# Kernel tuning notes

Measured on AMD Instinct MI355X. Metric: run time of the kernel, lower is better.

The kernel has to match this reference:

```python
import jax, jax.numpy as jnp
import numpy as np

T, WS, SHIFT, HEADS, DIM = 5, (8, 8), (4, 4), 6, 192
HEAD_DIM = DIM // HEADS
SCALE = HEAD_DIM ** -0.5
MLP_HID = 4 * DIM
TABLE_LEN = (T * 2 * WS[0] - 1) * (2 * WS[1] - 1)


def _rel_index():
    # exact replica of WindowAttention.__init__ index construction (t,h,w coords)
    ct, ch, cw = np.arange(T), np.arange(WS[0]), np.arange(WS[1])
    coords = np.stack(np.meshgrid(ct, ch, cw, indexing='ij')).reshape(3, -1)
    rel = (coords[:, :, None] - coords[:, None, :]).transpose(1, 2, 0).astype(np.int64)
    rel[:, :, 0] += WS[0] - 1
    rel[:, :, 1] += WS[1] - 1
    rel[:, :, 0] *= 2 * WS[1] - 1
    return jnp.asarray(rel.sum(-1))  # (N, N)


def _attn_mask(H, W):
    # standard shifted-window mask on (H,W); identical across T, so tile (T,T)
    img = np.zeros((H, W), np.float32)
    cnt = 0
    for hs in (slice(0, -WS[0]), slice(-WS[0], -SHIFT[0]), slice(-SHIFT[0], None)):
        for ws_ in (slice(0, -WS[1]), slice(-WS[1], -SHIFT[1]), slice(-SHIFT[1], None)):
            img[hs, ws_] = cnt
            cnt += 1
    img = img.reshape(H // WS[0], WS[0], W // WS[1], WS[1]).transpose(0, 2, 1, 3)
    img = img.reshape(-1, WS[0] * WS[1])  # (nW, Wh*Ww)
    m = img[:, None, :] - img[:, :, None]
    m = np.where(m != 0, -100.0, 0.0).astype(np.float32)
    return jnp.asarray(np.tile(m, (1, T, T)))  # (nW, T*Wh*Ww, T*Wh*Ww)


def _win_part(x, ws):
    B, t, H, W, C = x.shape
    x = x.reshape(B, t, H // ws[0], ws[0], W // ws[1], ws[1], C)
    return x.transpose(0, 2, 4, 1, 3, 5, 6).reshape(-1, t * ws[0] * ws[1], C)


def _win_rev(w, ws, H, W, t, B):
    x = w.reshape(B, H // ws[0], W // ws[1], t, ws[0], ws[1], -1)
    return x.transpose(0, 3, 1, 4, 2, 5, 6).reshape(B, t, H, W, -1)


def _ln(x, g, b):
    mu = x.mean(-1, keepdims=True)
    var = ((x - mu) ** 2).mean(-1, keepdims=True)
    return (x - mu) * jax.lax.rsqrt(var + 1e-5) * g + b


def _forward(x, ln1_g, ln1_b, qkv_w, qkv_b, rel_bias_table, proj_w, proj_b,
             ln2_g, ln2_b, fc1_w, fc1_b, fc2_w, fc2_b, H, W):
    B, L, C = x.shape
    shortcut = x
    h = _ln(x, ln1_g, ln1_b)
    qkv = h @ qkv_w.T + qkv_b                                   # (B, L, 3C)
    qkv = qkv.reshape(B, T, H, W, 3 * C)
    qkv = jnp.roll(qkv, (-SHIFT[0], -SHIFT[1]), axis=(2, 3))
    qkv = _win_part(qkv, WS)                                    # (B_, N, 3C)
    B_, N, _ = qkv.shape
    qkv = qkv.reshape(B_, N, 3, HEADS, HEAD_DIM).transpose(2, 0, 3, 1, 4)
    q, k, v = qkv[0], qkv[1], qkv[2]
    attn = jnp.einsum('bhnd,bhmd->bhnm', q * SCALE, k)          # (B_, H, N, N)
    bias = rel_bias_table[_rel_index()].transpose(2, 0, 1)      # (heads, N, N)
    attn = attn + bias[None]
    mask = _attn_mask(H, W)                                     # (nW, N, N)
    nW = mask.shape[0]
    attn = attn.reshape(B_ // nW, nW, HEADS, N, N) + mask[None, :, None]
    attn = jax.nn.softmax(attn.reshape(B_, HEADS, N, N), axis=-1)
    out = jnp.einsum('bhnm,bhmd->bhnd', attn, v)
    out = out.transpose(0, 2, 1, 3).reshape(B_, N, C)
    out = out @ proj_w.T + proj_b
    out = _win_rev(out, WS, H, W, T, B)
    out = jnp.roll(out, (SHIFT[0], SHIFT[1]), axis=(2, 3)).reshape(B, L, C)
    x = shortcut + out
    h = _ln(x, ln2_g, ln2_b)
    h = jax.nn.gelu(h @ fc1_w.T + fc1_b, approximate=False) @ fc2_w.T + fc2_b
    return x + h


def setup_inputs() -> dict:
    key = jax.random.key(0)
    ks = jax.random.split(key, 8)
    B, Himg, Wimg = 2, 64, 64
    L = T * Himg * Wimg
    s = 0.02
    return {
        'x': jax.random.normal(ks[0], (B, L, DIM), jnp.float32),
        'ln1_g': jnp.ones((DIM,), jnp.float32),
        'ln1_b': jnp.zeros((DIM,), jnp.float32),
        'qkv_w': jax.random.normal(ks[1], (3 * DIM, DIM), jnp.float32) * s,
        'qkv_b': jnp.zeros((3 * DIM,), jnp.float32),
        'rel_bias_table': jax.random.normal(ks[2], (TABLE_LEN, HEADS), jnp.float32) * s,
        'proj_w': jax.random.normal(ks[3], (DIM, DIM), jnp.float32) * s,
        'proj_b': jnp.zeros((DIM,), jnp.float32),
        'ln2_g': jnp.ones((DIM,), jnp.float32),
        'ln2_b': jnp.zeros((DIM,), jnp.float32),
        'fc1_w': jax.random.normal(ks[4], (MLP_HID, DIM), jnp.float32) * s,
        'fc1_b': jnp.zeros((MLP_HID,), jnp.float32),
        'fc2_w': jax.random.normal(ks[5], (DIM, MLP_HID), jnp.float32) * s,
        'fc2_b': jnp.zeros((DIM,), jnp.float32),
        'H': Himg,
        'W': Wimg,
    }


def reference(x, ln1_g, ln1_b, qkv_w, qkv_b, rel_bias_table, proj_w, proj_b,
              ln2_g, ln2_b, fc1_w, fc1_b, fc2_w, fc2_b, H, W):
    return _forward(x, ln1_g, ln1_b, qkv_w, qkv_b, rel_bias_table, proj_w, proj_b,
                    ln2_g, ln2_b, fc1_w, fc1_b, fc2_w, fc2_b, H, W)
```

## Files before the change

### kernel.cpp

```cpp
#include <hip/hip_runtime.h>
#include <math.h>

typedef unsigned short u16;
typedef unsigned int u32;
typedef short bf16x8 __attribute__((ext_vector_type(8)));
typedef float f32x4 __attribute__((ext_vector_type(4)));
typedef _Float16 f16x4 __attribute__((ext_vector_type(4)));

#define TT 5
#define HEADS 6
#define HD 32
#define DIM 192
#define NWIN 320
#define LTOK (TT*64*64)
#define BATCH 2
#define MROWS (BATCH*LTOK)
#define QSCALE 0.17677669529663687f
#define LOG2E 1.4426950408889634f
#define QSCALE2 (QSCALE * LOG2E)
#define MASK2 (-100.0f * LOG2E)

__device__ __forceinline__ u16 f2bf(float f) {
    u32 u = __float_as_uint(f);
    u32 r = (u + 0x7FFFu + ((u >> 16) & 1u)) >> 16;
    return (u16)r;
}
__device__ __forceinline__ float bflo(u32 u) { return __uint_as_float(u << 16); }
__device__ __forceinline__ float bfhi(u32 u) { return __uint_as_float(u & 0xFFFF0000u); }
__device__ __forceinline__ u32 pkh(float a, float b) {
    auto h = __builtin_amdgcn_cvt_pkrtz(a, b);
    return __builtin_bit_cast(u32, h);
}
#if __has_builtin(__builtin_amdgcn_exp2f)
__device__ __forceinline__ float ex2(float x) { return __builtin_amdgcn_exp2f(x); }
#else
__device__ __forceinline__ float ex2(float x) {
    float r; asm("v_exp_f32 %0, %1" : "=v"(r) : "v"(x)); return r;
}
#endif

__global__ __launch_bounds__(256) void cvt4_kernel(
    const float* __restrict__ a, const float* __restrict__ b,
    const float* __restrict__ c, const float* __restrict__ d,
    u16* __restrict__ oa, u16* __restrict__ ob,
    u16* __restrict__ oc, u16* __restrict__ od)
{
    int i = blockIdx.x * 256 + threadIdx.x;
    if (i < 110592)       oa[i]          = f2bf(a[i]);
    else if (i < 147456)  ob[i - 110592] = f2bf(b[i - 110592]);
    else if (i < 294912)  oc[i - 147456] = f2bf(c[i - 147456]);
    else                  od[i - 294912] = f2bf(d[i - 294912]);
}

__global__ __launch_bounds__(256) void ln_kernel(
    const float* __restrict__ x, const float* __restrict__ g,
    const float* __restrict__ b, u16* __restrict__ out)
{
    int tok  = blockIdx.x * 4 + (threadIdx.x >> 6);
    int lane = threadIdx.x & 63;
    const float* xr = x + (size_t)tok * DIM;
    float v0 = xr[lane], v1 = xr[lane + 64], v2 = xr[lane + 128];
    float s = v0 + v1 + v2;
    #pragma unroll
    for (int off = 32; off; off >>= 1) s += __shfl_xor(s, off, 64);
    float mu = s * (1.0f / 192.0f);
    float d0 = v0 - mu, d1 = v1 - mu, d2 = v2 - mu;
    float vs = d0 * d0 + d1 * d1 + d2 * d2;
    #pragma unroll
    for (int off = 32; off; off >>= 1) vs += __shfl_xor(vs, off, 64);
    float rstd = rsqrtf(vs * (1.0f / 192.0f) + 1e-5f);
    u16* orow = out + (size_t)tok * DIM;
    orow[lane]       = f2bf(d0 * rstd * g[lane]       + b[lane]);
    orow[lane + 64]  = f2bf(d1 * rstd * g[lane + 64]  + b[lane + 64]);
    orow[lane + 128] = f2bf(d2 * rstd * g[lane + 128] + b[lane + 128]);
}

template<int EPI, int BM>
__global__ __launch_bounds__(256) void mfma_gemm(
    const u16* __restrict__ A, const u16* __restrict__ W,
    const float* __restrict__ bias, void* __restrict__ outp,
    const float* __restrict__ xin, int N, int K)
{
    constexpr int WR = BM / 64;
    constexpr int NA = BM / 32;
    __shared__ u16 As[BM * 64];
    __shared__ u16 Bs[64 * 64];
    const int tid  = threadIdx.x;
    const int lane = tid & 63, wv = tid >> 6;
    const int ln16 = lane & 15, quad = lane >> 4;

    const int flat  = blockIdx.y * gridDim.x + blockIdx.x;
    const int cpx   = (gridDim.x * gridDim.y) >> 3;
    const int nf    = (flat & 7) * cpx + (flat >> 3);
    const int bn    = nf % gridDim.x;
    const int bm    = nf / gridDim.x;

    const int srow = lane >> 3;
    const int sxor = (lane & 7) ^ srow;
    const int acol = sxor * 8;

    f32x4 acc[WR][4] = {};

    for (int k0 = 0; k0 < K; k0 += 64) {
        __syncthreads();
        #pragma unroll
        for (int a = 0; a < NA; ++a) {
            const u16* g = A + (size_t)(bm * BM + a * 32 + wv * 8 + srow) * K + k0 + acol;
            __builtin_amdgcn_global_load_lds(
                (const __attribute__((address_space(1))) u32*)g,
                (__attribute__((address_space(3))) u32*)((char*)As + a * 4096 + wv * 1024),
                16, 0, 0);
        }
        #pragma unroll
        for (int bb = 0; bb < 2; ++bb) {
            const u16* g = W + (size_t)(bn * 64 + bb * 32 + wv * 8 + srow) * K + k0 + acol;
            __builtin_amdgcn_global_load_lds(
                (const __attribute__((address_space(1))) u32*)g,
                (__attribute__((address_space(3))) u32*)((char*)Bs + bb * 4096 + wv * 1024),
                16, 0, 0);
        }
        __syncthreads();
        #pragma unroll
        for (int s = 0; s < 2; ++s) {
            bf16x8 af[WR], bf[4];
            #pragma unroll
            for (int i = 0; i < WR; ++i) {
                int r = wv * (16 * WR) + i * 16 + ln16;
                int slot = (s * 4 + quad) ^ (r & 7);
                af[i] = *(const bf16x8*)((const char*)As + r * 128 + slot * 16);
            }
            #pragma unroll
            for (int j = 0; j < 4; ++j) {
                int r = j * 16 + ln16;
                int slot = (s * 4 + quad) ^ (r & 7);
                bf[j] = *(const bf16x8*)((const char*)Bs + r * 128 + slot * 16);
            }
            #pragma unroll
            for (int i = 0; i < WR; ++i)
                #pragma unroll
                for (int j = 0; j < 4; ++j)
                    acc[i][j] = __builtin_amdgcn_mfma_f32_16x16x32_bf16(
                        af[i], bf[j], acc[i][j], 0, 0, 0);
        }
    }

    #pragma unroll
    for (int i = 0; i < WR; ++i) {
        int gr0 = bm * BM + wv * (16 * WR) + i * 16 + quad * 4;
        #pragma unroll
        for (int j = 0; j < 4; ++j) {
            int gc = bn * 64 + j * 16 + ln16;
            float bv = bias[gc];
            #pragma unroll
            for (int rr = 0; rr < 4; ++rr) {
                int gr = gr0 + rr;
                float val = acc[i][j][rr] + bv;
                if (EPI == 0) {
                    ((u16*)outp)[(size_t)gr * N + gc] = f2bf(val);
                } else if (EPI == 1) {
                    float gl = val * 0.5f * (1.0f + erff(val * 0.70710678118654752f));
                    ((u16*)outp)[(size_t)gr * N + gc] = f2bf(gl);
                } else if (EPI == 2) {
                    int b_ = gr / NWIN, n = gr - b_ * NWIN;
                    int b = b_ >> 6, hb = (b_ >> 3) & 7, wb = b_ & 7;
                    int t = n >> 6, hi = (n >> 3) & 7, wj = n & 7;
                    int hs = (hb * 8 + hi + 4) & 63;
                    int wsrc = (wb * 8 + wj + 4) & 63;
                    size_t dst = ((size_t)b * LTOK + t * 4096 + hs * 64 + wsrc) * DIM + gc;
                    ((float*)outp)[dst] = xin[dst] + val;
                } else {
                    ((float*)outp)[(size_t)gr * N + gc] += val;
                }
            }
        }
    }
}

__global__ __launch_bounds__(320) void attn_kernel(
    const u16* __restrict__ qkv, const float* __restrict__ table,
    u16* __restrict__ attout)
{
    const int head = blockIdx.x % HEADS;
    const int b_   = blockIdx.x / HEADS;
    const int b = b_ >> 6, hb = (b_ >> 3) & 7, wb = b_ & 7;
    const int tid = threadIdx.x;
    const int lane = tid & 63, wv = tid >> 6;
    const int ln16 = lane & 15, quad = lane >> 4;

    __shared__ u16 Ks[320 * 40];
    __shared__ u16 Vt[32 * 328];
    __shared__ u16 meta[320];
    __shared__ float tbl[188];

    {
        int n = tid;
        int t1 = n >> 6, r1 = (n >> 3) & 7, c1 = n & 7;
        int h1 = hb * 8 + r1, w1 = wb * 8 + c1;
        int l1 = t1 * 4096 + ((h1 + 4) & 63) * 64 + ((w1 + 4) & 63);
        const u16* src = qkv + ((size_t)b * LTOK + l1) * (3 * DIM) + head * HD;
        const uint4* k4 = (const uint4*)(src + DIM);
        #pragma unroll
        for (int i = 0; i < 4; ++i)
            *(uint4*)(Ks + n * 40 + i * 8) = k4[i];
        const uint4* v4 = (const uint4*)(src + 2 * DIM);
        #pragma unroll
        for (int i = 0; i < 4; ++i) {
            uint4 u = v4[i];
            u32 ws[4] = {u.x, u.y, u.z, u.w};
            #pragma unroll
            for (int j = 0; j < 4; ++j) {
                u32 hb2 = pkh(bflo(ws[j]), bfhi(ws[j]));
                int d = i * 8 + j * 2;
                Vt[d * 328 + n]       = (u16)(hb2 & 0xFFFF);
                Vt[(d + 1) * 328 + n] = (u16)(hb2 >> 16);
            }
        }
        int off = (7 - t1) * 15 + 7 - r1 - c1;
        int rh = h1 < 56 ? 0 : (h1 < 60 ? 1 : 2);
        int rw = w1 < 56 ? 0 : (w1 < 60 ? 1 : 2);
        meta[n] = (u16)(off | ((rh * 3 + rw) << 8));
        if (n < 187) tbl[n] = table[n * HEADS + head] * LOG2E;
    }

    bf16x8 qf[4];
    int basen[4], myreg[4];
    #pragma unroll
    for (int qt = 0; qt < 4; ++qt) {
        int nq = wv * 64 + qt * 16 + ln16;
        int t1 = nq >> 6, r1 = (nq >> 3) & 7, c1 = nq & 7;
        int h1 = hb * 8 + r1, w1 = wb * 8 + c1;
        int l1 = t1 * 4096 + ((h1 + 4) & 63) * 64 + ((w1 + 4) & 63);
        qf[qt] = *(const bf16x8*)(qkv + ((size_t)b * LTOK + l1) * (3 * DIM)
                                  + head * HD + quad * 8);
        basen[qt] = t1 * 15 + r1 + c1;
        int rh = h1 < 56 ? 0 : (h1 < 60 ? 1 : 2);
        int rw = w1 < 56 ? 0 : (w1 < 60 ? 1 : 2);
        myreg[qt] = rh * 3 + rw;
    }

    __syncthreads();

    f32x4 o[4][2] = {};
    float l_[4] = {};
    const f32x4 zero = {};

    #pragma unroll 1
    for (int c = 0; c < 10; ++c) {
        int kb = c * 32;
        bf16x8 af0 = *(const bf16x8*)(Ks + (kb + ln16) * 40 + quad * 8);
        bf16x8 af1 = *(const bf16x8*)(Ks + (kb + 16 + ln16) * 40 + quad * 8);
        f16x4 va[2][2];
        #pragma unroll
        for (int dt = 0; dt < 2; ++dt)
            #pragma unroll
            for (int kt = 0; kt < 2; ++kt)
                va[dt][kt] = *(const f16x4*)(Vt + (dt * 16 + ln16) * 328
                                             + kb + kt * 16 + quad * 4);
        ushort4 m4a = *(const ushort4*)(meta + kb + quad * 4);
        ushort4 m4b = *(const ushort4*)(meta + kb + 16 + quad * 4);
        u16 mta[4] = {m4a.x, m4a.y, m4a.z, m4a.w};
        u16 mtb[4] = {m4b.x, m4b.y, m4b.z, m4b.w};

        #pragma unroll
        for (int qt = 0; qt < 4; ++qt) {
            f32x4 s0 = __builtin_amdgcn_mfma_f32_16x16x32_bf16(af0, qf[qt], zero, 0, 0, 0);
            f32x4 s1 = __builtin_amdgcn_mfma_f32_16x16x32_bf16(af1, qf[qt], zero, 0, 0, 0);
            float p[8];
            #pragma unroll
            for (int r = 0; r < 4; ++r) {
                int ma = mta[r], mb = mtb[r];
                float va0 = fmaf(s0[r], QSCALE2, tbl[basen[qt] + (ma & 0xFF)]);
                float vb0 = fmaf(s1[r], QSCALE2, tbl[basen[qt] + (mb & 0xFF)]);
                p[r]     = va0 + (((ma >> 8) == myreg[qt]) ? 0.0f : MASK2);
                p[4 + r] = vb0 + (((mb >> 8) == myreg[qt]) ? 0.0f : MASK2);
            }
            float ls = 0.0f;
            #pragma unroll
            for (int j = 0; j < 8; ++j) { p[j] = ex2(p[j]); ls += p[j]; }
            l_[qt] += ls;
            uint2 pk0 = { pkh(p[0], p[1]), pkh(p[2], p[3]) };
            uint2 pk1 = { pkh(p[4], p[5]), pkh(p[6], p[7]) };
            f16x4 pf0 = __builtin_bit_cast(f16x4, pk0);
            f16x4 pf1 = __builtin_bit_cast(f16x4, pk1);
            #pragma unroll
            for (int dt = 0; dt < 2; ++dt) {
                o[qt][dt] = __builtin_amdgcn_mfma_f32_16x16x16f16(va[dt][0], pf0, o[qt][dt], 0, 0, 0);
                o[qt][dt] = __builtin_amdgcn_mfma_f32_16x16x16f16(va[dt][1], pf1, o[qt][dt], 0, 0, 0);
            }
        }
    }

    #pragma unroll
    for (int qt = 0; qt < 4; ++qt) {
        float lt = l_[qt];
        lt += __shfl_xor(lt, 16, 64);
        lt += __shfl_xor(lt, 32, 64);
        float inv = 1.0f / lt;
        int nq = wv * 64 + qt * 16 + ln16;
        u16* dst = attout + ((size_t)(b_ * NWIN + nq)) * DIM + head * HD + quad * 4;
        #pragma unroll
        for (int dt = 0; dt < 2; ++dt) {
            u32 w0 = (u32)f2bf(o[qt][dt][0] * inv) | ((u32)f2bf(o[qt][dt][1] * inv) << 16);
            u32 w1 = (u32)f2bf(o[qt][dt][2] * inv) | ((u32)f2bf(o[qt][dt][3] * inv) << 16);
            uint2 st = {w0, w1};
            *(uint2*)(dst + dt * 16) = st;
        }
    }
}

extern "C" void kernel_launch(void* const* d_in, const int* in_sizes, int n_in,
                              void* d_out, int out_size, void* d_ws, size_t ws_size,
                              hipStream_t stream)
{
    (void)in_sizes; (void)n_in; (void)out_size; (void)ws_size;
    const float* x      = (const float*)d_in[0];
    const float* ln1_g  = (const float*)d_in[1];
    const float* ln1_b  = (const float*)d_in[2];
    const float* qkv_w  = (const float*)d_in[3];
    const float* qkv_b  = (const float*)d_in[4];
    const float* table  = (const float*)d_in[5];
    const float* proj_w = (const float*)d_in[6];
    const float* proj_b = (const float*)d_in[7];
    const float* ln2_g  = (const float*)d_in[8];
    const float* ln2_b  = (const float*)d_in[9];
    const float* fc1_w  = (const float*)d_in[10];
    const float* fc1_b  = (const float*)d_in[11];
    const float* fc2_w  = (const float*)d_in[12];
    const float* fc2_b  = (const float*)d_in[13];
    float* out = (float*)d_out;

    u16* wsu     = (u16*)d_ws;
    u16* h_buf   = wsu;
    u16* qkv_buf = wsu + (size_t)MROWS * DIM;
    u16* att_buf = wsu + (size_t)MROWS * (4 * DIM);
    u16* fc1_buf = wsu + (size_t)MROWS * DIM;
    u16* wq = wsu + (size_t)MROWS * (5 * DIM);
    u16* wp = wq + 3 * DIM * DIM;
    u16* w1 = wp + DIM * DIM;
    u16* w2 = w1 + 4 * DIM * DIM;

    cvt4_kernel<<<(12 * DIM * DIM) / 256, 256, 0, stream>>>(
        qkv_w, proj_w, fc1_w, fc2_w, wq, wp, w1, w2);

    ln_kernel<<<MROWS / 4, 256, 0, stream>>>(x, ln1_g, ln1_b, h_buf);
    mfma_gemm<0, 128><<<dim3(3 * DIM / 64, MROWS / 128), 256, 0, stream>>>(
        h_buf, wq, qkv_b, qkv_buf, nullptr, 3 * DIM, DIM);
    attn_kernel<<<128 * HEADS, 320, 0, stream>>>(qkv_buf, table, att_buf);
    mfma_gemm<2, 64><<<dim3(DIM / 64, MROWS / 64), 256, 0, stream>>>(
        att_buf, wp, proj_b, out, x, DIM, DIM);
    ln_kernel<<<MROWS / 4, 256, 0, stream>>>(out, ln2_g, ln2_b, h_buf);
    mfma_gemm<1, 128><<<dim3(4 * DIM / 64, MROWS / 128), 256, 0, stream>>>(
        h_buf, w1, fc1_b, fc1_buf, nullptr, 4 * DIM, DIM);
    mfma_gemm<3, 64><<<dim3(DIM / 64, MROWS / 64), 256, 0, stream>>>(
        fc1_buf, w2, fc2_b, out, nullptr, DIM, 4 * DIM);
}
```

Before: 252.8 us.

## Fuse fc1, GELU and fc2 into one MLP kernel keeping hidden activations on-chip

Replaces the two MLP GEMM launches with one fused kernel. Each 64-row block computes fc1 in chunks of 64 hidden units, applies bias and GELU in registers, packs the result to fp16, and accumulates fc2 straight into 12 output tiles. The 768-wide hidden activation no longer goes through global memory. The fc2 weights are now converted to fp16 so the second product can use the fp16 MFMA with register-resident A fragments. In exchange, every block reloads all of W1/W2 through LDS, the loop has little overlap since loads and compute are separated by barriers, and the two kernel launches become one.

```diff
diff --git a/kernel.cpp b/kernel.cpp
--- a/kernel.cpp
+++ b/kernel.cpp
@@ -49,7 +49,10 @@
     if (i < 110592)       oa[i]          = f2bf(a[i]);
     else if (i < 147456)  ob[i - 110592] = f2bf(b[i - 110592]);
     else if (i < 294912)  oc[i - 147456] = f2bf(c[i - 147456]);
-    else                  od[i - 294912] = f2bf(d[i - 294912]);
+    else {
+        _Float16 h = (_Float16)d[i - 294912];
+        od[i - 294912] = __builtin_bit_cast(u16, h);
+    }
 }
 
 __global__ __launch_bounds__(256) void ln_kernel(
@@ -157,9 +160,6 @@
                 float val = acc[i][j][rr] + bv;
                 if (EPI == 0) {
                     ((u16*)outp)[(size_t)gr * N + gc] = f2bf(val);
-                } else if (EPI == 1) {
-                    float gl = val * 0.5f * (1.0f + erff(val * 0.70710678118654752f));
-                    ((u16*)outp)[(size_t)gr * N + gc] = f2bf(gl);
                 } else if (EPI == 2) {
                     int b_ = gr / NWIN, n = gr - b_ * NWIN;
                     int b = b_ >> 6, hb = (b_ >> 3) & 7, wb = b_ & 7;
@@ -168,11 +168,124 @@
                     int wsrc = (wb * 8 + wj + 4) & 63;
                     size_t dst = ((size_t)b * LTOK + t * 4096 + hs * 64 + wsrc) * DIM + gc;
                     ((float*)outp)[dst] = xin[dst] + val;
-                } else {
-                    ((float*)outp)[(size_t)gr * N + gc] += val;
                 }
             }
         }
+    }
+}
+
+__global__ __launch_bounds__(256) void fused_mlp(
+    const u16* __restrict__ h,
+    const u16* __restrict__ w1,
+    const u16* __restrict__ w2f,
+    const float* __restrict__ b1,
+    const float* __restrict__ b2,
+    float* __restrict__ out)
+{
+    __shared__ u16 W1s[3 * 4096];
+    __shared__ u16 W2s[12288];
+    __shared__ float B1s[768];
+
+    const int tid  = threadIdx.x;
+    const int lane = tid & 63, wv = tid >> 6;
+    const int ln16 = lane & 15, quad = lane >> 4;
+    const int srow = lane >> 3;
+    const int acol = ((lane & 7) ^ srow) * 8;
+
+    const int flat = blockIdx.x;
+    const int bm   = (flat & 7) * (gridDim.x >> 3) + (flat >> 3);
+
+    B1s[tid]       = b1[tid];
+    if (tid < 256) { B1s[tid + 256] = b1[tid + 256]; B1s[tid + 512] = b1[tid + 512]; }
+
+    const u16* hrow = h + (size_t)(bm * 64 + wv * 16 + ln16) * DIM + quad * 8;
+    bf16x8 hf[3][2];
+    #pragma unroll
+    for (int c = 0; c < 3; ++c)
+        #pragma unroll
+        for (int s = 0; s < 2; ++s)
+            hf[c][s] = *(const bf16x8*)(hrow + c * 64 + s * 32);
+
+    f32x4 acc2[12] = {};
+
+    #pragma unroll 1
+    for (int nc = 0; nc < 12; ++nc) {
+        __syncthreads();
+        #pragma unroll
+        for (int c = 0; c < 3; ++c)
+            #pragma unroll
+            for (int bb = 0; bb < 2; ++bb) {
+                const u16* g = w1 + (size_t)(nc * 64 + bb * 32 + wv * 8 + srow) * DIM
+                               + c * 64 + acol;
+                __builtin_amdgcn_global_load_lds(
+                    (const __attribute__((address_space(1))) u32*)g,
+                    (__attribute__((address_space(3))) u32*)
+                        ((char*)W1s + c * 8192 + bb * 4096 + wv * 1024),
+                    16, 0, 0);
+            }
+        #pragma unroll
+        for (int bb = 0; bb < 6; ++bb) {
+            const u16* g = w2f + (size_t)(bb * 32 + wv * 8 + srow) * 768
+                           + nc * 64 + acol;
+            __builtin_amdgcn_global_load_lds(
+                (const __attribute__((address_space(1))) u32*)g,
+                (__attribute__((address_space(3))) u32*)
+                    ((char*)W2s + bb * 4096 + wv * 1024),
+                16, 0, 0);
+        }
+        __syncthreads();
+
+        f32x4 acc1[4] = {};
+        #pragma unroll
+        for (int c = 0; c < 3; ++c) {
+            #pragma unroll
+            for (int s = 0; s < 2; ++s) {
+                #pragma unroll
+                for (int kt = 0; kt < 4; ++kt) {
+                    int rw = kt * 16 + ln16;
+                    int slot = (s * 4 + quad) ^ (rw & 7);
+                    bf16x8 wa = *(const bf16x8*)((const char*)W1s + c * 8192 + rw * 128 + slot * 16);
+                    acc1[kt] = __builtin_amdgcn_mfma_f32_16x16x32_bf16(
+                        wa, hf[c][s], acc1[kt], 0, 0, 0);
+                }
+            }
+        }
+
+        f16x4 pf[4];
+        #pragma unroll
+        for (int kt = 0; kt < 4; ++kt) {
+            const float* bp = B1s + nc * 64 + kt * 16 + quad * 4;
+            float gv[4];
+            #pragma unroll
+            for (int rr = 0; rr < 4; ++rr) {
+                float v = acc1[kt][rr] + bp[rr];
+                gv[rr] = v * 0.5f * (1.0f + erff(v * 0.70710678118654752f));
+            }
+            uint2 pk = { pkh(gv[0], gv[1]), pkh(gv[2], gv[3]) };
+            pf[kt] = __builtin_bit_cast(f16x4, pk);
+        }
+
+        #pragma unroll
+        for (int kt = 0; kt < 4; ++kt) {
+            #pragma unroll
+            for (int nt = 0; nt < 12; ++nt) {
+                int rn = nt * 16 + ln16;
+                int slot = (kt * 2 + (quad >> 1)) ^ (rn & 7);
+                f16x4 wb = *(const f16x4*)((const char*)W2s + rn * 128 + slot * 16 + (quad & 1) * 8);
+                acc2[nt] = __builtin_amdgcn_mfma_f32_16x16x16f16(
+                    pf[kt], wb, acc2[nt], 0, 0, 0);
+            }
+        }
+    }
+
+    #pragma unroll
+    for (int nt = 0; nt < 12; ++nt) {
+        int gc = nt * 16 + ln16;
+        float bv = b2[gc];
+        int gr0 = bm * 64 + wv * 16 + quad * 4;
+        #pragma unroll
+        for (int rr = 0; rr < 4; ++rr)
+            out[(size_t)(gr0 + rr) * DIM + gc] += acc2[nt][rr] + bv;
     }
 }
 
@@ -333,7 +446,6 @@
     u16* h_buf   = wsu;
     u16* qkv_buf = wsu + (size_t)MROWS * DIM;
     u16* att_buf = wsu + (size_t)MROWS * (4 * DIM);
-    u16* fc1_buf = wsu + (size_t)MROWS * DIM;
     u16* wq = wsu + (size_t)MROWS * (5 * DIM);
     u16* wp = wq + 3 * DIM * DIM;
     u16* w1 = wp + DIM * DIM;
@@ -349,8 +461,6 @@
     mfma_gemm<2, 64><<<dim3(DIM / 64, MROWS / 64), 256, 0, stream>>>(
         att_buf, wp, proj_b, out, x, DIM, DIM);
     ln_kernel<<<MROWS / 4, 256, 0, stream>>>(out, ln2_g, ln2_b, h_buf);
-    mfma_gemm<1, 128><<<dim3(4 * DIM / 64, MROWS / 128), 256, 0, stream>>>(
-        h_buf, w1, fc1_b, fc1_buf, nullptr, 4 * DIM, DIM);
-    mfma_gemm<3, 64><<<dim3(DIM / 64, MROWS / 64), 256, 0, stream>>>(
-        fc1_buf, w2, fc2_b, out, nullptr, DIM, 4 * DIM);
-}
+    fused_mlp<<<MROWS / 64, 256, 0, stream>>>(
+        h_buf, w1, w2, fc1_b, fc2_b, out);
+}
```

Result: slower. 284.2 us (+12.4%).
